# Kernel optimization log

Hardware: AMD Instinct MI355X
Metric: run time of the kernel (lower is better)

The kernel has to match this reference:

```python
import jax, jax.numpy as jnp
import numpy as np

KSIZE = 3   # patch kernel
NSIZE = 7   # search neighborhood
SCALE = 4   # downscale factor
ALPHA = 1


def _patches(x, k, pad_mode):
    # x: [b,c,h,w] -> [b, c*k*k, h, w], feature ordering channel-major
    # (matches torch.nn.functional.unfold ordering).
    if pad_mode == 'reflect':
        p = k // 2
        xp = jnp.pad(x, ((0, 0), (0, 0), (p, p), (p, p)), mode='reflect')
        return jax.lax.conv_general_dilated_patches(xp, (k, k), (1, 1), 'VALID')
    return jax.lax.conv_general_dilated_patches(x, (k, k), (1, 1), 'SAME')


def census(x):
    # UFlow-style soft census transform (the CensusTransform used in this repo):
    # grayscale*255, 3x3 zero-padded patches minus center, soft-sign normalize.
    gray = (0.299 * x[:, 0:1] + 0.587 * x[:, 1:2] + 0.114 * x[:, 2:3]) * 255.0
    p = _patches(gray, KSIZE, 'zero')          # [b, 9, h, w]
    t = p - gray
    return t / jnp.sqrt(0.81 + t * t)


def downsample(x):
    b, c, h, w = x.shape
    return jax.image.resize(x, (b, c, h // SCALE, w // SCALE), method='cubic')


def unfold_center(x):
    # _unfold(data, with_unfold=False): [b,c,h,w] -> [b, hw, c*k*k]
    x = downsample(x)
    b, c, h, w = x.shape
    p = _patches(x, KSIZE, 'reflect').reshape(b, c * KSIZE * KSIZE, h * w)
    return p.transpose(0, 2, 1)


def unfold_nbr(x):
    # _unfold(data, with_unfold=True): [b,c,h,w] -> [b, hw, n*n, c*k*k]
    x = downsample(x)
    b, c, h, w = x.shape
    d1 = _patches(x, KSIZE, 'reflect')          # [b, c*k*k, h, w]
    c1 = d1.shape[1]
    d2 = _patches(d1, NSIZE, 'reflect')         # [b, c1*n*n, h, w]
    d2 = d2.reshape(b, c1, NSIZE * NSIZE, h * w)
    return d2.transpose(0, 3, 2, 1)


def reference(pred, I):
    # --- census-space distance + argmin over 2*n*n candidates ---
    p_ct = unfold_center(census(pred))                       # [b, hw, 81]
    nbr_ct = jnp.concatenate(
        [unfold_nbr(census(I[:, 0])), unfold_nbr(census(I[:, 1]))], axis=2
    )                                                        # [b, hw, 2n^2, 81]
    # ||p - n||^2 expanded as p2 + n2 - 2 p.n (avoids the huge repeated diff)
    p2 = jnp.sum(p_ct * p_ct, axis=-1)                       # [b, hw]
    n2 = jnp.sum(nbr_ct * nbr_ct, axis=-1)                   # [b, hw, 2n^2]
    dis = p2[:, :, None] + n2 - 2.0 * jnp.einsum('bpc,bpnc->bpn', p_ct, nbr_ct)
    ind = jnp.argmin(dis, axis=2)                            # [b, hw]
    # --- gather matched raw patches and compute loss ---
    p = unfold_center(pred)                                  # [b, hw, 27]
    nbr = jnp.concatenate(
        [unfold_nbr(I[:, 0]), unfold_nbr(I[:, 1])], axis=2
    )                                                        # [b, hw, 2n^2, 27]
    matched = jnp.take_along_axis(nbr, ind[:, :, None, None], axis=2)[:, :, 0]
    return jnp.mean((p - matched) ** 2 * 0.5)


def setup_inputs() -> dict:
    key = jax.random.key(0)
    k1, k2 = jax.random.split(key)
    pred = jax.random.normal(k1, (2, 3, 384, 384), dtype=jnp.float32)
    I = jax.random.normal(k2, (2, 2, 3, 384, 384), dtype=jnp.float32)
    return {'pred': pred, 'I': I}
```

## Files before the change

kernel.cpp:

```cpp
#include <hip/hip_runtime.h>
#include <math.h>

#define FH 384
#define FW 384
#define DH 96
#define DW 96
#define NIMG 6
#define PLANE (DH * DW)
#define NPIX (2 * PLANE)

__device__ __forceinline__ float keysc(float x) {
    if (x < 1.f) return ((1.5f * x - 2.5f) * x) * x + 1.f;
    if (x < 2.f) return ((-0.5f * x + 2.5f) * x - 4.f) * x + 2.f;
    return 0.f;
}

__device__ __forceinline__ int refl(int i, int n) {
    if (i < 0) i = -i;
    if (i >= n) i = 2 * (n - 1) - i;
    return i;
}

__device__ __forceinline__ int clampi(int i) { return min(max(i, 0), 95); }

__global__ void k_gray(const float* __restrict__ pred, const float* __restrict__ I,
                       float* __restrict__ gray) {
    int idx = blockIdx.x * 256 + threadIdx.x;
    const int total = NIMG * FH * FW;
    if (idx >= total) return;
    int img = idx / (FH * FW);
    int px  = idx % (FH * FW);
    const float* src;
    if (img < 2) {
        src = pred + img * 3 * FH * FW;
    } else {
        int j = (img - 2) >> 1, b = (img - 2) & 1;
        src = I + ((b * 2 + j) * 3) * FH * FW;
    }
    float r = src[px], g = src[FH * FW + px], b = src[2 * FH * FW + px];
    gray[idx] = (0.299f * r + 0.587f * g + 0.114f * b) * 255.0f;
}

__global__ void k_census_downH(const float* __restrict__ gray, float* __restrict__ CH) {
    int idx = blockIdx.x * 256 + threadIdx.x;
    const int total = NIMG * 9 * DH * FW;
    if (idx >= total) return;
    int x  = idx % FW;
    int t1 = idx / FW;
    int yo = t1 % DH;
    int t2 = t1 / DH;
    int k  = t2 % 9;
    int img = t2 / 9;
    int dy = k / 3 - 1, dx = k % 3 - 1;
    const float* g = gray + img * FH * FW;
    float acc = 0.f, z = 0.f;
#pragma unroll
    for (int t = 0; t < 16; ++t) {
        int r = 4 * yo - 6 + t;
        if (r < 0 || r >= FH) continue;
        float w = keysc(fabsf((float)t - 7.5f) * 0.25f);
        z += w;
        float gc = g[r * FW + x];
        int r2 = r + dy, c2 = x + dx;
        float gn = (r2 < 0 || r2 >= FH || c2 < 0 || c2 >= FW) ? 0.f : g[r2 * FW + c2];
        float tt = gn - gc;
        acc += w * (tt / sqrtf(0.81f + tt * tt));
    }
    CH[idx] = acc / z;
}

__global__ void k_downW(const float* __restrict__ src, float* __restrict__ dst, int nrows) {
    int idx = blockIdx.x * 256 + threadIdx.x;
    int total = nrows * DW;
    if (idx >= total) return;
    int xo = idx % DW;
    int row = idx / DW;
    const float* s = src + row * FW;
    float acc = 0.f, z = 0.f;
#pragma unroll
    for (int t = 0; t < 16; ++t) {
        int i = 4 * xo - 6 + t;
        if (i < 0 || i >= FW) continue;
        float w = keysc(fabsf((float)t - 7.5f) * 0.25f);
        z += w;
        acc += w * s[i];
    }
    dst[idx] = acc / z;
}

__global__ void k_raw_downH(const float* __restrict__ pred, const float* __restrict__ I,
                            float* __restrict__ RH) {
    int idx = blockIdx.x * 256 + threadIdx.x;
    const int total = NIMG * 3 * DH * FW;
    if (idx >= total) return;
    int x  = idx % FW;
    int t1 = idx / FW;
    int yo = t1 % DH;
    int t2 = t1 / DH;
    int c  = t2 % 3;
    int img = t2 / 3;
    const float* src;
    if (img < 2) {
        src = pred + (img * 3 + c) * FH * FW;
    } else {
        int j = (img - 2) >> 1, b = (img - 2) & 1;
        src = I + (((b * 2 + j) * 3) + c) * FH * FW;
    }
    float acc = 0.f, z = 0.f;
#pragma unroll
    for (int t = 0; t < 16; ++t) {
        int r = 4 * yo - 6 + t;
        if (r < 0 || r >= FH) continue;
        float w = keysc(fabsf((float)t - 7.5f) * 0.25f);
        z += w;
        acc += w * src[r * FW + x];
    }
    RH[idx] = acc / z;
}

__global__ void k_n2(const float* __restrict__ CD, float* __restrict__ N2) {
    int idx = blockIdx.x * 256 + threadIdx.x;
    if (idx >= 4 * PLANE) return;
    int img4 = idx / PLANE;
    int pos  = idx % PLANE;
    int y = pos / DW, x = pos % DW;
    int ry[3], rx[3];
#pragma unroll
    for (int kk = 0; kk < 3; ++kk) {
        ry[kk] = refl(y + kk - 1, DH);
        rx[kk] = refl(x + kk - 1, DW);
    }
    const float* C = CD + (2 + img4) * 9 * PLANE;
    float s = 0.f;
#pragma unroll
    for (int c = 0; c < 9; ++c)
#pragma unroll
        for (int ky = 0; ky < 3; ++ky)
#pragma unroll
            for (int kx = 0; kx < 3; ++kx) {
                float v = C[c * PLANE + ry[ky] * DW + rx[kx]];
                s += v * v;
            }
    N2[idx] = s;
}

__global__ __launch_bounds__(256) void k_match(const float* __restrict__ CD,
                                               const float* __restrict__ N2,
                                               const float* __restrict__ RD,
                                               float* __restrict__ partial) {
    __shared__ float nb[2][9][9][40];
    __shared__ float ct[9][3][34];
    __shared__ float sbd[256];
    __shared__ int   sbn[256];
    __shared__ float red[32];

    int bid = blockIdx.x;
    int b   = bid / 288;
    int rem = bid % 288;
    int y   = rem / 3;
    int x0  = (rem % 3) * 32;

    int px = threadIdx.x & 31;
    int g  = threadIdx.x >> 5;
    int x  = x0 + px;

    for (int idx = threadIdx.x; idx < 2 * 9 * 9 * 40; idx += 256) {
        int j   = idx / 3240;
        int r1  = idx % 3240;
        int c   = r1 / 360;
        int r2  = r1 % 360;
        int u   = r2 / 40;
        int v   = r2 % 40;
        int gy  = clampi(y - 4 + u);
        int gx  = clampi(x0 - 4 + v);
        nb[j][c][u][v] = CD[((2 + 2 * j + b) * 9 + c) * PLANE + gy * DW + gx];
    }
    for (int idx = threadIdx.x; idx < 9 * 3 * 34; idx += 256) {
        int c = idx / 102;
        int r1 = idx % 102;
        int u = r1 / 34;
        int v = r1 % 34;
        int gy = clampi(y - 1 + u);
        int gx = clampi(x0 - 1 + v);
        ct[c][u][v] = CD[(b * 9 + c) * PLANE + gy * DW + gx];
    }
    __syncthreads();

    int cy_s[3], cx_s[3];
#pragma unroll
    for (int kk = 0; kk < 3; ++kk) {
        cy_s[kk] = refl(y + kk - 1, DH) - (y - 1);
        cx_s[kk] = refl(x + kk - 1, DW) - (x0 - 1);
    }

    float best = INFINITY;
    int bn = 1 << 30;
    for (int k = 0; k < 13; ++k) {
        int n = 8 * k + g;
        if (n >= 98) break;
        int j = n / 49, rr = n % 49;
        int dy = rr / 7 - 3, dx = rr % 7 - 3;
        int yy = refl(y + dy, DH), xx = refl(x + dx, DW);
        int ry_s[3], rx_s[3];
#pragma unroll
        for (int kk = 0; kk < 3; ++kk) {
            ry_s[kk] = refl(yy + kk - 1, DH) - (y - 4);
            rx_s[kk] = refl(xx + kk - 1, DW) - (x0 - 4);
        }
        float dot = 0.f;
#pragma unroll
        for (int c = 0; c < 9; ++c)
#pragma unroll
            for (int ky = 0; ky < 3; ++ky)
#pragma unroll
                for (int kx = 0; kx < 3; ++kx)
                    dot += ct[c][cy_s[ky]][cx_s[kx]] * nb[j][c][ry_s[ky]][rx_s[kx]];
        float dis = N2[(2 * j + b) * PLANE + yy * DW + xx] - 2.f * dot;
        if (dis < best) { best = dis; bn = n; }
    }
    sbd[threadIdx.x] = best;
    sbn[threadIdx.x] = bn;
    __syncthreads();

    float loss = 0.f;
    if (g == 0) {
        float d0 = sbd[px];
        int   n0 = sbn[px];
#pragma unroll
        for (int gg = 1; gg < 8; ++gg) {
            float d = sbd[gg * 32 + px];
            int   n = sbn[gg * 32 + px];
            if (d < d0 || (d == d0 && n < n0)) { d0 = d; n0 = n; }
        }
        int j = n0 / 49, rr = n0 % 49;
        int dy = rr / 7 - 3, dx = rr % 7 - 3;
        int yy = refl(y + dy, DH), xx = refl(x + dx, DW);
        int ry0[3], rx0[3], ry[3], rx[3];
#pragma unroll
        for (int kk = 0; kk < 3; ++kk) {
            ry0[kk] = refl(y + kk - 1, DH);
            rx0[kk] = refl(x + kk - 1, DW);
            ry[kk]  = refl(yy + kk - 1, DH);
            rx[kk]  = refl(xx + kk - 1, DW);
        }
        const float* RDp = RD + b * 3 * PLANE;
        const float* RDn = RD + (2 + 2 * j + b) * 3 * PLANE;
#pragma unroll
        for (int c = 0; c < 3; ++c)
#pragma unroll
            for (int ky = 0; ky < 3; ++ky)
#pragma unroll
                for (int kx = 0; kx < 3; ++kx) {
                    float a = RDp[c * PLANE + ry0[ky] * DW + rx0[kx]];
                    float m = RDn[c * PLANE + ry[ky] * DW + rx[kx]];
                    float d = a - m;
                    loss += d * d;
                }
        red[px] = loss;
    }
    __syncthreads();
    if (threadIdx.x == 0) {
        float s = 0.f;
#pragma unroll
        for (int i = 0; i < 32; ++i) s += red[i];
        partial[bid] = s;
    }
}

#define NPART 576
__global__ void k_final(const float* __restrict__ partial, float* __restrict__ out) {
    __shared__ float red[256];
    float v = 0.f;
    for (int i = threadIdx.x; i < NPART; i += 256) v += partial[i];
    red[threadIdx.x] = v;
    __syncthreads();
#pragma unroll
    for (int s = 128; s > 0; s >>= 1) {
        if (threadIdx.x < s) red[threadIdx.x] += red[threadIdx.x + s];
        __syncthreads();
    }
    if (threadIdx.x == 0) out[0] = red[0] * (0.5f / 497664.0f);
}

extern "C" void kernel_launch(void* const* d_in, const int* in_sizes, int n_in,
                              void* d_out, int out_size, void* d_ws, size_t ws_size,
                              hipStream_t stream) {
    const float* pred = (const float*)d_in[0];
    const float* I    = (const float*)d_in[1];
    float* out = (float*)d_out;
    float* ws  = (float*)d_ws;

    float* CD   = ws;
    float* RD   = CD + 497664;
    float* S    = RD + 165888;
    float* gray = S;
    float* CH   = S + 884736;
    float* RH   = CH + 1990656;
    float* N2   = S;
    float* part = S + 36864;

    k_gray<<<(NIMG * FH * FW + 255) / 256, 256, 0, stream>>>(pred, I, gray);
    k_census_downH<<<(NIMG * 9 * DH * FW + 255) / 256, 256, 0, stream>>>(gray, CH);
    k_raw_downH<<<(NIMG * 3 * DH * FW + 255) / 256, 256, 0, stream>>>(pred, I, RH);
    k_downW<<<((NIMG * 12 * DH) * DW + 255) / 256, 256, 0, stream>>>(CH, CD, NIMG * 12 * DH);
    k_n2<<<(4 * PLANE + 255) / 256, 256, 0, stream>>>(CD, N2);
    k_match<<<576, 256, 0, stream>>>(CD, N2, RD, part);
    k_final<<<1, 256, 0, stream>>>(part, out);
}
```

Before: 141.3 us.

## Compute all nine census channels per thread and cache center patch in registers

The census vertical-downsample kernel now has each thread produce all 9 census offsets for one output position. It slides a 3-row register window instead of launching one thread per offset, which removes redundant gray loads and index math and writes the always-zero center channel directly. The match kernel preloads the 81-element center patch into registers once rather than re-reading it from shared memory for every candidate, and sets launch_bounds occupancy to 1 block per SM. The larger register footprint may lower occupancy in k_match.

```diff
diff --git a/kernel.cpp b/kernel.cpp
--- a/kernel.cpp
+++ b/kernel.cpp
@@ -22,6 +22,10 @@
 }
 
 __device__ __forceinline__ int clampi(int i) { return min(max(i, 0), 95); }
+
+__device__ __forceinline__ float softsign(float t) {
+    return t / sqrtf(0.81f + t * t);
+}
 
 __global__ void k_gray(const float* __restrict__ pred, const float* __restrict__ I,
                        float* __restrict__ gray) {
@@ -41,32 +45,66 @@
     gray[idx] = (0.299f * r + 0.587f * g + 0.114f * b) * 255.0f;
 }
 
-__global__ void k_census_downH(const float* __restrict__ gray, float* __restrict__ CH) {
-    int idx = blockIdx.x * 256 + threadIdx.x;
-    const int total = NIMG * 9 * DH * FW;
+__global__ __launch_bounds__(256) void k_census_downH(const float* __restrict__ gray,
+                                                      float* __restrict__ CH) {
+    int idx = blockIdx.x * 256 + threadIdx.x;
+    const int total = NIMG * DH * FW;
     if (idx >= total) return;
-    int x  = idx % FW;
-    int t1 = idx / FW;
-    int yo = t1 % DH;
-    int t2 = t1 / DH;
-    int k  = t2 % 9;
-    int img = t2 / 9;
-    int dy = k / 3 - 1, dx = k % 3 - 1;
+    int x   = idx % FW;
+    int t1  = idx / FW;
+    int yo  = t1 % DH;
+    int img = t1 / DH;
     const float* g = gray + img * FH * FW;
-    float acc = 0.f, z = 0.f;
+
+    bool xl = (x > 0), xr = (x < FW - 1);
+
+    float a0, a1, a2, b0, b1, b2, c0, c1, c2;
+    auto loadrow = [&](int r, float& v0, float& v1, float& v2) {
+        if (r < 0 || r >= FH) { v0 = v1 = v2 = 0.f; return; }
+        const float* gr = g + r * FW + x;
+        v1 = gr[0];
+        v0 = xl ? gr[-1] : 0.f;
+        v2 = xr ? gr[1] : 0.f;
+    };
+
+    int rbase = 4 * yo - 6;
+    loadrow(rbase - 1, a0, a1, a2);
+    loadrow(rbase,     b0, b1, b2);
+
+    float acc0 = 0.f, acc1 = 0.f, acc2 = 0.f, acc3 = 0.f, acc5 = 0.f,
+          acc6 = 0.f, acc7 = 0.f, acc8 = 0.f, z = 0.f;
 #pragma unroll
     for (int t = 0; t < 16; ++t) {
-        int r = 4 * yo - 6 + t;
-        if (r < 0 || r >= FH) continue;
-        float w = keysc(fabsf((float)t - 7.5f) * 0.25f);
-        z += w;
-        float gc = g[r * FW + x];
-        int r2 = r + dy, c2 = x + dx;
-        float gn = (r2 < 0 || r2 >= FH || c2 < 0 || c2 >= FW) ? 0.f : g[r2 * FW + c2];
-        float tt = gn - gc;
-        acc += w * (tt / sqrtf(0.81f + tt * tt));
-    }
-    CH[idx] = acc / z;
+        int r = rbase + t;
+        loadrow(r + 1, c0, c1, c2);
+        if (r >= 0 && r < FH) {
+            float w = keysc(fabsf((float)t - 7.5f) * 0.25f);
+            z += w;
+            float gc = b1;
+            acc0 += w * softsign(a0 - gc);
+            acc1 += w * softsign(a1 - gc);
+            acc2 += w * softsign(a2 - gc);
+            acc3 += w * softsign(b0 - gc);
+            acc5 += w * softsign(b2 - gc);
+            acc6 += w * softsign(c0 - gc);
+            acc7 += w * softsign(c1 - gc);
+            acc8 += w * softsign(c2 - gc);
+        }
+        a0 = b0; a1 = b1; a2 = b2;
+        b0 = c0; b1 = c1; b2 = c2;
+    }
+    float inv = 1.f / z;
+    float* o = CH + (img * 9 * DH + yo) * FW + x;
+    const int STR = DH * FW;
+    o[0 * STR] = acc0 * inv;
+    o[1 * STR] = acc1 * inv;
+    o[2 * STR] = acc2 * inv;
+    o[3 * STR] = acc3 * inv;
+    o[4 * STR] = 0.f;
+    o[5 * STR] = acc5 * inv;
+    o[6 * STR] = acc6 * inv;
+    o[7 * STR] = acc7 * inv;
+    o[8 * STR] = acc8 * inv;
 }
 
 __global__ void k_downW(const float* __restrict__ src, float* __restrict__ dst, int nrows) {
@@ -144,10 +182,10 @@
     N2[idx] = s;
 }
 
-__global__ __launch_bounds__(256) void k_match(const float* __restrict__ CD,
-                                               const float* __restrict__ N2,
-                                               const float* __restrict__ RD,
-                                               float* __restrict__ partial) {
+__global__ __launch_bounds__(256, 1) void k_match(const float* __restrict__ CD,
+                                                  const float* __restrict__ N2,
+                                                  const float* __restrict__ RD,
+                                                  float* __restrict__ partial) {
     __shared__ float nb[2][9][9][40];
     __shared__ float ct[9][3][34];
     __shared__ float sbd[256];
@@ -192,6 +230,14 @@
         cy_s[kk] = refl(y + kk - 1, DH) - (y - 1);
         cx_s[kk] = refl(x + kk - 1, DW) - (x0 - 1);
     }
+    float p[81];
+#pragma unroll
+    for (int c = 0; c < 9; ++c)
+#pragma unroll
+        for (int ky = 0; ky < 3; ++ky)
+#pragma unroll
+            for (int kx = 0; kx < 3; ++kx)
+                p[c * 9 + ky * 3 + kx] = ct[c][cy_s[ky]][cx_s[kx]];
 
     float best = INFINITY;
     int bn = 1 << 30;
@@ -214,7 +260,7 @@
             for (int ky = 0; ky < 3; ++ky)
 #pragma unroll
                 for (int kx = 0; kx < 3; ++kx)
-                    dot += ct[c][cy_s[ky]][cx_s[kx]] * nb[j][c][ry_s[ky]][rx_s[kx]];
+                    dot += p[c * 9 + ky * 3 + kx] * nb[j][c][ry_s[ky]][rx_s[kx]];
         float dis = N2[(2 * j + b) * PLANE + yy * DW + xx] - 2.f * dot;
         if (dis < best) { best = dis; bn = n; }
     }
@@ -222,7 +268,6 @@
     sbn[threadIdx.x] = bn;
     __syncthreads();
 
-    float loss = 0.f;
     if (g == 0) {
         float d0 = sbd[px];
         int   n0 = sbn[px];
@@ -245,6 +290,7 @@
         }
         const float* RDp = RD + b * 3 * PLANE;
         const float* RDn = RD + (2 + 2 * j + b) * 3 * PLANE;
+        float loss = 0.f;
 #pragma unroll
         for (int c = 0; c < 3; ++c)
 #pragma unroll
@@ -300,7 +346,7 @@
     float* part = S + 36864;
 
     k_gray<<<(NIMG * FH * FW + 255) / 256, 256, 0, stream>>>(pred, I, gray);
-    k_census_downH<<<(NIMG * 9 * DH * FW + 255) / 256, 256, 0, stream>>>(gray, CH);
+    k_census_downH<<<(NIMG * DH * FW + 255) / 256, 256, 0, stream>>>(gray, CH);
     k_raw_downH<<<(NIMG * 3 * DH * FW + 255) / 256, 256, 0, stream>>>(pred, I, RH);
     k_downW<<<((NIMG * 12 * DH) * DW + 255) / 256, 256, 0, stream>>>(CH, CD, NIMG * 12 * DH);
     k_n2<<<(4 * PLANE + 255) / 256, 256, 0, stream>>>(CD, N2);
```

New measurement: 134.7 us. 4.7% less time.

## Split match kernel per neighbor frame and hoist center patch into registers

Applied to the files above, without the earlier changes.

The match kernel now runs one block per (frame j, batch, row segment), which doubles the grid to 1152 blocks and halves the neighbor tile in shared memory. Each thread caches its 81-element center census patch in registers instead of rereading it from LDS for every candidate. A new combine kernel merges the two per-frame argmins with the same tie-breaking rule, gathers the raw patches and reduces the loss. The aim is more parallelism and less LDS traffic, at the cost of an extra launch, a round trip through global memory for intermediates, and register pressure from the 81-float array under launch_bounds(256,1).

```diff
diff --git a/kernel.cpp b/kernel.cpp
--- a/kernel.cpp
+++ b/kernel.cpp
@@ -144,19 +144,20 @@
     N2[idx] = s;
 }
 
-__global__ __launch_bounds__(256) void k_match(const float* __restrict__ CD,
-                                               const float* __restrict__ N2,
-                                               const float* __restrict__ RD,
-                                               float* __restrict__ partial) {
-    __shared__ float nb[2][9][9][40];
+__global__ __launch_bounds__(256, 1) void k_match(const float* __restrict__ CD,
+                                                  const float* __restrict__ N2,
+                                                  float* __restrict__ bestd,
+                                                  int* __restrict__ bestn) {
+    __shared__ float nb[9][9][40];
     __shared__ float ct[9][3][34];
     __shared__ float sbd[256];
     __shared__ int   sbn[256];
-    __shared__ float red[32];
 
     int bid = blockIdx.x;
-    int b   = bid / 288;
-    int rem = bid % 288;
+    int j   = bid / 576;
+    int sub = bid % 576;
+    int b   = sub / 288;
+    int rem = sub % 288;
     int y   = rem / 3;
     int x0  = (rem % 3) * 32;
 
@@ -164,22 +165,20 @@
     int g  = threadIdx.x >> 5;
     int x  = x0 + px;
 
-    for (int idx = threadIdx.x; idx < 2 * 9 * 9 * 40; idx += 256) {
-        int j   = idx / 3240;
-        int r1  = idx % 3240;
-        int c   = r1 / 360;
-        int r2  = r1 % 360;
-        int u   = r2 / 40;
-        int v   = r2 % 40;
-        int gy  = clampi(y - 4 + u);
-        int gx  = clampi(x0 - 4 + v);
-        nb[j][c][u][v] = CD[((2 + 2 * j + b) * 9 + c) * PLANE + gy * DW + gx];
+    for (int idx = threadIdx.x; idx < 9 * 9 * 40; idx += 256) {
+        int c  = idx / 360;
+        int r2 = idx % 360;
+        int u  = r2 / 40;
+        int v  = r2 % 40;
+        int gy = clampi(y - 4 + u);
+        int gx = clampi(x0 - 4 + v);
+        nb[c][u][v] = CD[((2 + 2 * j + b) * 9 + c) * PLANE + gy * DW + gx];
     }
     for (int idx = threadIdx.x; idx < 9 * 3 * 34; idx += 256) {
-        int c = idx / 102;
+        int c  = idx / 102;
         int r1 = idx % 102;
-        int u = r1 / 34;
-        int v = r1 % 34;
+        int u  = r1 / 34;
+        int v  = r1 % 34;
         int gy = clampi(y - 1 + u);
         int gx = clampi(x0 - 1 + v);
         ct[c][u][v] = CD[(b * 9 + c) * PLANE + gy * DW + gx];
@@ -192,37 +191,47 @@
         cy_s[kk] = refl(y + kk - 1, DH) - (y - 1);
         cx_s[kk] = refl(x + kk - 1, DW) - (x0 - 1);
     }
+    float p[81];
+#pragma unroll
+    for (int c = 0; c < 9; ++c)
+#pragma unroll
+        for (int ky = 0; ky < 3; ++ky)
+#pragma unroll
+            for (int kx = 0; kx < 3; ++kx)
+                p[c * 9 + ky * 3 + kx] = ct[c][cy_s[ky]][cx_s[kx]];
+#pragma unroll
+    for (int f = 0; f < 81; ++f) asm volatile("" : "+v"(p[f]));
 
     float best = INFINITY;
     int bn = 1 << 30;
-    for (int k = 0; k < 13; ++k) {
-        int n = 8 * k + g;
-        if (n >= 98) break;
-        int j = n / 49, rr = n % 49;
-        int dy = rr / 7 - 3, dx = rr % 7 - 3;
-        int yy = refl(y + dy, DH), xx = refl(x + dx, DW);
-        int ry_s[3], rx_s[3];
-#pragma unroll
-        for (int kk = 0; kk < 3; ++kk) {
-            ry_s[kk] = refl(yy + kk - 1, DH) - (y - 4);
-            rx_s[kk] = refl(xx + kk - 1, DW) - (x0 - 4);
+#pragma unroll
+    for (int k = 0; k < 7; ++k) {
+        int rr = 8 * k + g;
+        if (rr < 49) {
+            int dy = rr / 7 - 3, dx = rr % 7 - 3;
+            int yy = refl(y + dy, DH), xx = refl(x + dx, DW);
+            int ry_s[3], rx_s[3];
+#pragma unroll
+            for (int kk = 0; kk < 3; ++kk) {
+                ry_s[kk] = refl(yy + kk - 1, DH) - (y - 4);
+                rx_s[kk] = refl(xx + kk - 1, DW) - (x0 - 4);
+            }
+            float dot = 0.f;
+#pragma unroll
+            for (int c = 0; c < 9; ++c)
+#pragma unroll
+                for (int ky = 0; ky < 3; ++ky)
+#pragma unroll
+                    for (int kx = 0; kx < 3; ++kx)
+                        dot += p[c * 9 + ky * 3 + kx] * nb[c][ry_s[ky]][rx_s[kx]];
+            float dis = N2[(2 * j + b) * PLANE + yy * DW + xx] - 2.f * dot;
+            if (dis < best) { best = dis; bn = j * 49 + rr; }
         }
-        float dot = 0.f;
-#pragma unroll
-        for (int c = 0; c < 9; ++c)
-#pragma unroll
-            for (int ky = 0; ky < 3; ++ky)
-#pragma unroll
-                for (int kx = 0; kx < 3; ++kx)
-                    dot += ct[c][cy_s[ky]][cx_s[kx]] * nb[j][c][ry_s[ky]][rx_s[kx]];
-        float dis = N2[(2 * j + b) * PLANE + yy * DW + xx] - 2.f * dot;
-        if (dis < best) { best = dis; bn = n; }
     }
     sbd[threadIdx.x] = best;
     sbn[threadIdx.x] = bn;
     __syncthreads();
 
-    float loss = 0.f;
     if (g == 0) {
         float d0 = sbd[px];
         int   n0 = sbn[px];
@@ -232,50 +241,72 @@
             int   n = sbn[gg * 32 + px];
             if (d < d0 || (d == d0 && n < n0)) { d0 = d; n0 = n; }
         }
-        int j = n0 / 49, rr = n0 % 49;
-        int dy = rr / 7 - 3, dx = rr % 7 - 3;
-        int yy = refl(y + dy, DH), xx = refl(x + dx, DW);
-        int ry0[3], rx0[3], ry[3], rx[3];
-#pragma unroll
-        for (int kk = 0; kk < 3; ++kk) {
-            ry0[kk] = refl(y + kk - 1, DH);
-            rx0[kk] = refl(x + kk - 1, DW);
-            ry[kk]  = refl(yy + kk - 1, DH);
-            rx[kk]  = refl(xx + kk - 1, DW);
-        }
-        const float* RDp = RD + b * 3 * PLANE;
-        const float* RDn = RD + (2 + 2 * j + b) * 3 * PLANE;
-#pragma unroll
-        for (int c = 0; c < 3; ++c)
-#pragma unroll
-            for (int ky = 0; ky < 3; ++ky)
-#pragma unroll
-                for (int kx = 0; kx < 3; ++kx) {
-                    float a = RDp[c * PLANE + ry0[ky] * DW + rx0[kx]];
-                    float m = RDn[c * PLANE + ry[ky] * DW + rx[kx]];
-                    float d = a - m;
-                    loss += d * d;
-                }
-        red[px] = loss;
-    }
+        int pid = b * PLANE + y * DW + x;
+        bestd[j * NPIX + pid] = d0;
+        bestn[j * NPIX + pid] = n0;
+    }
+}
+
+__global__ __launch_bounds__(256) void k_combine(const float* __restrict__ bestd,
+                                                 const int* __restrict__ bestn,
+                                                 const float* __restrict__ RD,
+                                                 float* __restrict__ partial) {
+    int pid = blockIdx.x * 256 + threadIdx.x;
+    int b   = pid / PLANE;
+    int pos = pid % PLANE;
+    int y = pos / DW, x = pos % DW;
+
+    float d0 = bestd[pid];
+    int   n0 = bestn[pid];
+    float d1 = bestd[NPIX + pid];
+    int   n1 = bestn[NPIX + pid];
+    if (d1 < d0 || (d1 == d0 && n1 < n0)) { d0 = d1; n0 = n1; }
+
+    int j = n0 / 49, rr = n0 % 49;
+    int dy = rr / 7 - 3, dx = rr % 7 - 3;
+    int yy = refl(y + dy, DH), xx = refl(x + dx, DW);
+    int ry0[3], rx0[3], ry[3], rx[3];
+#pragma unroll
+    for (int kk = 0; kk < 3; ++kk) {
+        ry0[kk] = refl(y + kk - 1, DH);
+        rx0[kk] = refl(x + kk - 1, DW);
+        ry[kk]  = refl(yy + kk - 1, DH);
+        rx[kk]  = refl(xx + kk - 1, DW);
+    }
+    const float* RDp = RD + b * 3 * PLANE;
+    const float* RDn = RD + (2 + 2 * j + b) * 3 * PLANE;
+    float loss = 0.f;
+#pragma unroll
+    for (int c = 0; c < 3; ++c)
+#pragma unroll
+        for (int ky = 0; ky < 3; ++ky)
+#pragma unroll
+            for (int kx = 0; kx < 3; ++kx) {
+                float a = RDp[c * PLANE + ry0[ky] * DW + rx0[kx]];
+                float m = RDn[c * PLANE + ry[ky] * DW + rx[kx]];
+                float d = a - m;
+                loss += d * d;
+            }
+
+    __shared__ float red[256];
+    red[threadIdx.x] = loss;
     __syncthreads();
-    if (threadIdx.x == 0) {
-        float s = 0.f;
-#pragma unroll
-        for (int i = 0; i < 32; ++i) s += red[i];
-        partial[bid] = s;
-    }
-}
-
-#define NPART 576
+#pragma unroll
+    for (int s = 128; s > 0; s >>= 1) {
+        if (threadIdx.x < s) red[threadIdx.x] += red[threadIdx.x + s];
+        __syncthreads();
+    }
+    if (threadIdx.x == 0) partial[blockIdx.x] = red[0];
+}
+
+#define NPART 72
 __global__ void k_final(const float* __restrict__ partial, float* __restrict__ out) {
-    __shared__ float red[256];
-    float v = 0.f;
-    for (int i = threadIdx.x; i < NPART; i += 256) v += partial[i];
+    __shared__ float red[128];
+    float v = (threadIdx.x < NPART) ? partial[threadIdx.x] : 0.f;
     red[threadIdx.x] = v;
     __syncthreads();
 #pragma unroll
-    for (int s = 128; s > 0; s >>= 1) {
+    for (int s = 64; s > 0; s >>= 1) {
         if (threadIdx.x < s) red[threadIdx.x] += red[threadIdx.x + s];
         __syncthreads();
     }
@@ -297,13 +328,16 @@
     float* CH   = S + 884736;
     float* RH   = CH + 1990656;
     float* N2   = S;
-    float* part = S + 36864;
+    float* bestd = S + 36864;
+    int*   bestn = (int*)(S + 73728);
+    float* part  = S + 110592;
 
     k_gray<<<(NIMG * FH * FW + 255) / 256, 256, 0, stream>>>(pred, I, gray);
     k_census_downH<<<(NIMG * 9 * DH * FW + 255) / 256, 256, 0, stream>>>(gray, CH);
     k_raw_downH<<<(NIMG * 3 * DH * FW + 255) / 256, 256, 0, stream>>>(pred, I, RH);
     k_downW<<<((NIMG * 12 * DH) * DW + 255) / 256, 256, 0, stream>>>(CH, CD, NIMG * 12 * DH);
     k_n2<<<(4 * PLANE + 255) / 256, 256, 0, stream>>>(CD, N2);
-    k_match<<<576, 256, 0, stream>>>(CD, N2, RD, part);
-    k_final<<<1, 256, 0, stream>>>(part, out);
-}
+    k_match<<<1152, 256, 0, stream>>>(CD, N2, bestd, bestn);
+    k_combine<<<NPIX / 256, 256, 0, stream>>>(bestd, bestn, RD, part);
+    k_final<<<1, 128, 0, stream>>>(part, out);
+}
```

Result: no change. 140.8 us (-0.3%).
